# Performance work log

Measured on AMD Instinct MI355X. Metric: run time of the kernel, lower is better.

The kernel has to match this reference:

```python
import jax, jax.numpy as jnp
import numpy as np

# Powderworld element-id mapping (channel 0 holds the element id as a float)
ELEM = {'empty': 0, 'sand': 1, 'water': 3, 'wall': 2, 'plant': 5, 'stone': 6,
        'lava': 8, 'gas': 9, 'wood': 7, 'ice': 10, 'fire': 11, 'dust': 13,
        'acid': 12, 'cloner': 4, 'agentKangaroo': 14, 'agentLemming': 15}
NUM_ELEMS = 16
B, C, H, W = 16, 20, 512, 512


def _get_bool(world, name):
    return world[:, 0:1] == ELEM[name]


def _roll_left(x):
    return jnp.roll(x, shift=1, axis=3)


def _roll_right(x):
    return jnp.roll(x, shift=-1, axis=3)


def setup_inputs() -> dict:
    key = jax.random.key(0)
    k1, k2, k3, k4, k5, k6, k7 = jax.random.split(key, 7)
    world = jax.random.normal(k1, (B, C, H, W), dtype=jnp.float32) * 0.1
    # channel 0: element ids; channel 2: gravity flag in {0,1}; channel 8: did-gravity flag
    ids = jax.random.randint(k2, (B, 1, H, W), 0, NUM_ELEMS).astype(jnp.float32)
    grav = jax.random.bernoulli(k3, 0.8, (B, 1, H, W)).astype(jnp.float32)
    didg = jax.random.bernoulli(k4, 0.2, (B, 1, H, W)).astype(jnp.float32)
    world = world.at[:, 0:1].set(ids).at[:, 2:3].set(grav).at[:, 8:9].set(didg)
    rand_movement = jax.random.uniform(k5, (B, 1, H, W), dtype=jnp.float32)
    rand_interact = jax.random.uniform(k6, (B, 1, H, W), dtype=jnp.float32)
    rand_element = jax.random.uniform(k7, (B, 1, H, W), dtype=jnp.float32)
    return {'world': world, 'rand_movement': rand_movement,
            'rand_interact': rand_interact, 'rand_element': rand_element}


def reference(world, rand_movement, rand_interact, rand_element):
    f32 = world.dtype
    new_fluid_momentum = jnp.zeros_like(world[:, 0:1])
    for fall_left in (True, False):
        get_in_dir = _roll_left if fall_left else _roll_right
        get_in_not_dir = _roll_right if fall_left else _roll_left
        fall_dir = (rand_movement + world[:, 6:7] + new_fluid_momentum) > 0.5
        is_matching_fall = fall_dir if fall_left else ~fall_dir
        world_left = get_in_dir(world)
        world_right = get_in_not_dir(world)
        is_air_move = _get_bool(world, 'agentKangaroo') | _get_bool(world, 'agentLemming')
        is_element = (_get_bool(world, 'empty') | _get_bool(world, 'water')
                      | _get_bool(world, 'gas') | _get_bool(world, 'lava')
                      | _get_bool(world, 'acid') | is_air_move)
        is_left_density_lower = (world[:, 1:2] - world_left[:, 1:2]) > 0
        is_gravity = world[:, 2:3] == 1
        is_left_gravity = world_left[:, 2:3] == 1
        not_did_gravity_left = (~(world[:, 8:9] > 0)) | is_air_move
        does_become_left = (is_matching_fall & is_element & not_did_gravity_left
                            & is_left_density_lower & is_left_gravity & is_gravity)
        does_become_right = get_in_not_dir(does_become_left)
        has_overlap = does_become_left & does_become_right
        does_become_left_real = does_become_left & ~has_overlap
        does_become_right_real = get_in_not_dir(does_become_left_real)
        new_fluid_momentum = new_fluid_momentum + does_become_right_real.astype(f32) * (2.0 if fall_left else -2.0)
        # interp2: (~a & ~b)*world + a*world_left + b*world_right
        a = does_become_left_real.astype(f32)
        b = does_become_right_real.astype(f32)
        neither = (~does_become_left_real & ~does_become_right_real).astype(f32)
        world = neither * world + a * world_left + b * world_right
    is_fluid = (_get_bool(world, 'empty') | _get_bool(world, 'water')
                | _get_bool(world, 'gas') | _get_bool(world, 'lava')
                | _get_bool(world, 'acid') | _get_bool(world, 'agentKangaroo')
                | _get_bool(world, 'agentLemming'))
    mom = jnp.where(is_fluid, new_fluid_momentum, world[:, 6:7])
    world = world.at[:, 6:7].set(mom)
    return world
```

## Files before the change

kernel.cpp:

```cpp
#include <hip/hip_runtime.h>


#define WW 512
#define HH 512
#define CC 20
#define BB 16

__device__ __forceinline__ bool is_fluid_id(float id) {
    return (id == 0.0f) | (id == 3.0f) | (id == 9.0f) | (id == 8.0f) |
           (id == 12.0f) | (id == 14.0f) | (id == 15.0f);
}

__global__ __launch_bounds__(512)
void fluid_flow_kernel(const float* __restrict__ world,
                       const float* __restrict__ rand_movement,
                       float* __restrict__ out) {
    __shared__ float id_s[WW];
    __shared__ float den_s[WW];
    __shared__ float grav_s[WW];
    __shared__ float mom_s[WW];
    __shared__ float didg_s[WW];
    __shared__ float rm_s[WW];
    __shared__ int   dbl_s[WW];
    __shared__ int   s1_s[WW];

    const int row = blockIdx.x;
    const int b   = row >> 9;
    const int h   = row & (HH - 1);
    const int x   = threadIdx.x;

    const size_t planeHW = (size_t)HH * WW;
    const size_t baseRow = ((size_t)b * CC * HH + (size_t)h) * WW;

    id_s[x]   = world[baseRow + 0 * planeHW + x];
    den_s[x]  = world[baseRow + 1 * planeHW + x];
    grav_s[x] = world[baseRow + 2 * planeHW + x];
    mom_s[x]  = world[baseRow + 6 * planeHW + x];
    didg_s[x] = world[baseRow + 8 * planeHW + x];
    rm_s[x]   = rand_movement[((size_t)b * HH + (size_t)h) * WW + x];
    __syncthreads();

    {
        const float fd  = rm_s[x] + mom_s[x];
        const bool matching = fd > 0.5f;
        const float idc = id_s[x];
        const bool ia = (idc == 14.0f) | (idc == 15.0f);
        const bool ie = (idc == 0.0f) | (idc == 3.0f) | (idc == 9.0f) |
                        (idc == 8.0f) | (idc == 12.0f) | ia;
        const int  xl  = (x - 1) & (WW - 1);
        const bool ldl = (den_s[x] - den_s[xl]) > 0.0f;
        const bool ig  = grav_s[x]  == 1.0f;
        const bool ilg = grav_s[xl] == 1.0f;
        const bool ndg = (!(didg_s[x] > 0.0f)) | ia;
        dbl_s[x] = (matching & ie & ndg & ldl & ilg & ig) ? 1 : 0;
    }
    __syncthreads();

    float nfm;
    {
        const int d0 = dbl_s[x];
        const int d1 = dbl_s[(x + 1) & (WW - 1)];
        const int d2 = dbl_s[(x + 2) & (WW - 1)];
        const bool a1 = d0 && !d1;
        const bool b1 = d1 && !d2;
        s1_s[x] = a1 ? ((x - 1) & (WW - 1)) : (b1 ? ((x + 1) & (WW - 1)) : x);
        nfm = b1 ? 2.0f : 0.0f;
    }
    __syncthreads();

    {
        const int c = s1_s[x];
        const int l = s1_s[(x + 1) & (WW - 1)];
        const float fd = (rm_s[x] + mom_s[c]) + nfm;
        const bool matching = !(fd > 0.5f);
        const float idc = id_s[c];
        const bool ia = (idc == 14.0f) | (idc == 15.0f);
        const bool ie = (idc == 0.0f) | (idc == 3.0f) | (idc == 9.0f) |
                        (idc == 8.0f) | (idc == 12.0f) | ia;
        const bool ldl = (den_s[c] - den_s[l]) > 0.0f;
        const bool ig  = grav_s[c] == 1.0f;
        const bool ilg = grav_s[l] == 1.0f;
        const bool ndg = (!(didg_s[c] > 0.0f)) | ia;
        const bool d = matching & ie & ndg & ldl & ilg & ig;
        __syncthreads();
        dbl_s[x] = d ? 1 : 0;
    }
    __syncthreads();

    int   sx;
    float nfm_final;
    {
        const int d0  = dbl_s[x];
        const int dm1 = dbl_s[(x - 1) & (WW - 1)];
        const int dm2 = dbl_s[(x - 2) & (WW - 1)];
        const bool a2 = d0  && !dm1;
        const bool b2 = dm1 && !dm2;
        const int s2  = a2 ? ((x + 1) & (WW - 1)) : (b2 ? ((x - 1) & (WW - 1)) : x);
        sx = s1_s[s2];
        nfm_final = nfm + (b2 ? -2.0f : 0.0f);
    }

    const float fid   = id_s[sx];
    const bool  fluid = is_fluid_id(fid);

    out[baseRow + 0 * planeHW + x] = fid;
    out[baseRow + 1 * planeHW + x] = den_s[sx];
    out[baseRow + 2 * planeHW + x] = grav_s[sx];
    out[baseRow + 6 * planeHW + x] = fluid ? nfm_final : mom_s[sx];
    out[baseRow + 8 * planeHW + x] = didg_s[sx];

    #pragma unroll
    for (int c = 0; c < CC; ++c) {
        if (c == 0 || c == 1 || c == 2 || c == 6 || c == 8) continue;
        out[baseRow + (size_t)c * planeHW + x] = world[baseRow + (size_t)c * planeHW + sx];
    }
}

extern "C" void kernel_launch(void* const* d_in, const int* in_sizes, int n_in,
                              void* d_out, int out_size, void* d_ws, size_t ws_size,
                              hipStream_t stream) {
    const float* world = (const float*)d_in[0];
    const float* rm    = (const float*)d_in[1];
    float* out = (float*)d_out;

    dim3 grid(BB * HH);
    dim3 block(WW);
    fluid_flow_kernel<<<grid, block, 0, stream>>>(world, rm, out);
}
```

Baseline: 553.1 us.

## Vectorize row loads and stage channel permutation through shared memory

New measurement: 554.9 us. No clear change (+0.3%).

```diff
diff --git a/kernel.cpp b/kernel.cpp
--- a/kernel.cpp
+++ b/kernel.cpp
@@ -15,29 +15,48 @@
 void fluid_flow_kernel(const float* __restrict__ world,
                        const float* __restrict__ rand_movement,
                        float* __restrict__ out) {
-    __shared__ float id_s[WW];
-    __shared__ float den_s[WW];
-    __shared__ float grav_s[WW];
-    __shared__ float mom_s[WW];
-    __shared__ float didg_s[WW];
-    __shared__ float rm_s[WW];
+    __shared__ __attribute__((aligned(16))) float id_s[WW];
+    __shared__ __attribute__((aligned(16))) float den_s[WW];
+    __shared__ __attribute__((aligned(16))) float grav_s[WW];
+    __shared__ __attribute__((aligned(16))) float mom_s[WW];
+    __shared__ __attribute__((aligned(16))) float didg_s[WW];
+    __shared__ __attribute__((aligned(16))) float rm_s[WW];
+    __shared__ __attribute__((aligned(16))) float momout_s[WW];
     __shared__ int   dbl_s[WW];
     __shared__ int   s1_s[WW];
+    __shared__ short sfin_s[WW];
+    __shared__ __attribute__((aligned(16))) float buf[2][4][WW];
 
     const int row = blockIdx.x;
     const int b   = row >> 9;
     const int h   = row & (HH - 1);
     const int x   = threadIdx.x;
 
-    const size_t planeHW = (size_t)HH * WW;
+    const size_t plane   = (size_t)HH * WW;
     const size_t baseRow = ((size_t)b * CC * HH + (size_t)h) * WW;
+    const size_t rrow    = ((size_t)b * HH + (size_t)h) * WW;
 
-    id_s[x]   = world[baseRow + 0 * planeHW + x];
-    den_s[x]  = world[baseRow + 1 * planeHW + x];
-    grav_s[x] = world[baseRow + 2 * planeHW + x];
-    mom_s[x]  = world[baseRow + 6 * planeHW + x];
-    didg_s[x] = world[baseRow + 8 * planeHW + x];
-    rm_s[x]   = rand_movement[((size_t)b * HH + (size_t)h) * WW + x];
+    {
+        int f = x;
+        #pragma unroll
+        for (int it = 0; it < 2; ++it, f += 512) {
+            if (f < 768) {
+                const int a  = f >> 7;
+                const int q4 = f & 127;
+                const float4* sp;
+                float* dp;
+                switch (a) {
+                    case 0: sp = (const float4*)(world + baseRow);             dp = id_s;   break;
+                    case 1: sp = (const float4*)(world + baseRow + plane);     dp = den_s;  break;
+                    case 2: sp = (const float4*)(world + baseRow + 2 * plane); dp = grav_s; break;
+                    case 3: sp = (const float4*)(world + baseRow + 6 * plane); dp = mom_s;  break;
+                    case 4: sp = (const float4*)(world + baseRow + 8 * plane); dp = didg_s; break;
+                    default: sp = (const float4*)(rand_movement + rrow);       dp = rm_s;   break;
+                }
+                ((float4*)dp)[q4] = sp[q4];
+            }
+        }
+    }
     __syncthreads();
 
     {
@@ -87,8 +106,6 @@
     }
     __syncthreads();
 
-    int   sx;
-    float nfm_final;
     {
         const int d0  = dbl_s[x];
         const int dm1 = dbl_s[(x - 1) & (WW - 1)];
@@ -96,23 +113,39 @@
         const bool a2 = d0  && !dm1;
         const bool b2 = dm1 && !dm2;
         const int s2  = a2 ? ((x + 1) & (WW - 1)) : (b2 ? ((x - 1) & (WW - 1)) : x);
-        sx = s1_s[s2];
-        nfm_final = nfm + (b2 ? -2.0f : 0.0f);
+        const int sx  = s1_s[s2];
+        const float nfm_final = nfm + (b2 ? -2.0f : 0.0f);
+        const bool fluid = is_fluid_id(id_s[sx]);
+        momout_s[x] = fluid ? nfm_final : mom_s[sx];
+        sfin_s[x]   = (short)sx;
     }
+    __syncthreads();
 
-    const float fid   = id_s[sx];
-    const bool  fluid = is_fluid_id(fid);
-
-    out[baseRow + 0 * planeHW + x] = fid;
-    out[baseRow + 1 * planeHW + x] = den_s[sx];
-    out[baseRow + 2 * planeHW + x] = grav_s[sx];
-    out[baseRow + 6 * planeHW + x] = fluid ? nfm_final : mom_s[sx];
-    out[baseRow + 8 * planeHW + x] = didg_s[sx];
+    const int slot = x >> 7;
+    const int q    = x & 127;
 
     #pragma unroll
-    for (int c = 0; c < CC; ++c) {
-        if (c == 0 || c == 1 || c == 2 || c == 6 || c == 8) continue;
-        out[baseRow + (size_t)c * planeHW + x] = world[baseRow + (size_t)c * planeHW + sx];
+    for (int g = 0; g < 5; ++g) {
+        const int c = 4 * g + slot;
+        float* bslot = buf[g & 1][slot];
+
+        float4 v;
+        if      (c == 0) v = ((const float4*)id_s)[q];
+        else if (c == 1) v = ((const float4*)den_s)[q];
+        else if (c == 2) v = ((const float4*)grav_s)[q];
+        else if (c == 6) v = ((const float4*)momout_s)[q];
+        else if (c == 8) v = ((const float4*)didg_s)[q];
+        else             v = *(const float4*)(world + baseRow + (size_t)c * plane + 4 * q);
+        ((float4*)bslot)[q] = v;
+        __syncthreads();
+
+        float* op = out + baseRow + (size_t)c * plane;
+        #pragma unroll
+        for (int j = 0; j < 4; ++j) {
+            const int m   = q + 128 * j;
+            const int src = (c == 6) ? m : (int)sfin_s[m];
+            op[m] = bslot[src];
+        }
     }
 }
 
```
